# Kernel tuning notes

Hardware: AMD Instinct MI355X
Metric: run time of the kernel (lower is better)

Reference implementation:

```python
import jax, jax.numpy as jnp
import numpy as np

IN_FEATURES = 4096
OUT_FEATURES = 16384
B, S = 8, 16  # small token count -> weight-traffic bound (decode-like)


def setup_inputs() -> dict:
    key = jax.random.key(0)
    k_x, k_w, k_b = jax.random.split(key, 3)
    x = jax.random.normal(k_x, (B, S, IN_FEATURES), dtype=jnp.float32)
    # symmetric int8 quantized weight, values in [-127, 127]
    weight_int = jax.random.randint(k_w, (OUT_FEATURES, IN_FEATURES), -127, 128, dtype=jnp.int32)
    weight_scale = jnp.float32(0.01)      # scalar scale (symmetric, per-tensor)
    weight_zero_point = jnp.float32(0.0)  # symmetric -> zero_point = 0
    bias = jax.random.normal(k_b, (OUT_FEATURES,), dtype=jnp.float32)
    return {"x": x, "weight_int": weight_int, "weight_scale": weight_scale,
            "weight_zero_point": weight_zero_point, "bias": bias}


def reference(x, weight_int, weight_scale, weight_zero_point, bias):
    # dequantize: (q - zp) * scale, then F.linear: x @ W^T + b
    weight_float = (weight_int.astype(jnp.float32) - weight_zero_point) * weight_scale
    # x: [B, S, in], weight_float: [out, in] -> [B, S, out]
    return jnp.einsum('bsi,oi->bso', x, weight_float) + bias
```

## Files before the change

kernel.cpp:

```cpp
#include <hip/hip_runtime.h>
#include <hip/hip_bf16.h>


#define IN_F 4096
#define OUT_F 16384
#define NTOK 128

typedef __attribute__((ext_vector_type(8))) short bf16x8;
typedef __attribute__((ext_vector_type(4))) float f32x4;

__device__ __forceinline__ unsigned short f32_to_bf16_rne(float f) {
  unsigned u = __float_as_uint(f);
  u += 0x7fffu + ((u >> 16) & 1u);
  return (unsigned short)(u >> 16);
}

__global__ __launch_bounds__(512) void prep_x(const float* __restrict__ x,
                                              uint4* __restrict__ xf,
                                              float* __restrict__ xsum) {
  const int token = blockIdx.x;
  const int i = (int)threadIdx.x;
  const int k0 = i << 3;
  const float4 v0 = *(const float4*)(x + token * IN_F + k0);
  const float4 v1 = *(const float4*)(x + token * IN_F + k0 + 4);
  float v[8] = {v0.x, v0.y, v0.z, v0.w, v1.x, v1.y, v1.z, v1.w};
  unsigned short h[8];
  float s = 0.f;
#pragma unroll
  for (int j = 0; j < 8; ++j) {
    s += v[j];
    h[j] = f32_to_bf16_rne(v[j]);
  }
  uint4 o;
  o.x = (unsigned)h[0] | ((unsigned)h[1] << 16);
  o.y = (unsigned)h[2] | ((unsigned)h[3] << 16);
  o.z = (unsigned)h[4] | ((unsigned)h[5] << 16);
  o.w = (unsigned)h[6] | ((unsigned)h[7] << 16);
  const int slab = i >> 2;
  const int q = i & 3;
  const int lane = (q << 4) | (token & 15);
  xf[slab * 512 + (token >> 4) * 64 + lane] = o;

#pragma unroll
  for (int off = 32; off > 0; off >>= 1) s += __shfl_down(s, off, 64);
  __shared__ float wsum[8];
  if ((i & 63) == 0) wsum[i >> 6] = s;
  __syncthreads();
  if (i == 0) {
    float t = 0.f;
#pragma unroll
    for (int a = 0; a < 8; ++a) t += wsum[a];
    xsum[token] = t;
  }
}

__device__ __forceinline__ bf16x8 cvt8(int4 a, int4 b) {
  bf16x8 o;
  o[0] = (short)(__float_as_uint((float)a.x) >> 16);
  o[1] = (short)(__float_as_uint((float)a.y) >> 16);
  o[2] = (short)(__float_as_uint((float)a.z) >> 16);
  o[3] = (short)(__float_as_uint((float)a.w) >> 16);
  o[4] = (short)(__float_as_uint((float)b.x) >> 16);
  o[5] = (short)(__float_as_uint((float)b.y) >> 16);
  o[6] = (short)(__float_as_uint((float)b.z) >> 16);
  o[7] = (short)(__float_as_uint((float)b.w) >> 16);
  return o;
}

__global__ __launch_bounds__(64, 1) void qlinear_main(
    const int* __restrict__ W, const uint4* __restrict__ xf,
    const float* __restrict__ xsum, const float* __restrict__ scale_p,
    const float* __restrict__ zp_p, const float* __restrict__ bias,
    float* __restrict__ out) {
  const int l = (int)threadIdx.x;
  const int q = l >> 4;
  const int r = l & 15;
  const int rt = (int)blockIdx.x;
  const int R0 = rt * 16;

  const int* Wbase = W + (R0 + r) * IN_F + q * 8;
  const int start = (rt * 37) & 127;

  int4 wa[8], wb[8];
  uint4 bb[2][8];

  f32x4 acc[8];
#pragma unroll
  for (int t = 0; t < 8; ++t) acc[t] = (f32x4)0.0f;

#pragma unroll
  for (int d = 0; d < 8; ++d) {
    const int kk = (start + d) & 127;
    wa[d] = *(const int4*)(Wbase + kk * 32);
    wb[d] = *(const int4*)(Wbase + kk * 32 + 4);
  }
#pragma unroll
  for (int d = 0; d < 2; ++d) {
    const int kk = (start + d) & 127;
    const uint4* xp = xf + kk * 512 + l;
#pragma unroll
    for (int t = 0; t < 8; ++t) bb[d][t] = xp[t * 64];
  }

#pragma unroll 1
  for (int k = 0; k <= 112; k += 8) {
#pragma unroll
    for (int u = 0; u < 8; ++u) {
      const int step = k + u;
      {
        const int kk = (start + step + 2) & 127;
        const uint4* xp = xf + kk * 512 + l;
        uint4 nb0 = xp[0 * 64], nb1 = xp[1 * 64], nb2 = xp[2 * 64], nb3 = xp[3 * 64];
        uint4 nb4 = xp[4 * 64], nb5 = xp[5 * 64], nb6 = xp[6 * 64], nb7 = xp[7 * 64];
        const int kw = (start + step + 8) & 127;
        int4 nwa = *(const int4*)(Wbase + kw * 32);
        int4 nwb = *(const int4*)(Wbase + kw * 32 + 4);
        bf16x8 a = cvt8(wa[u], wb[u]);
        wa[u] = nwa;
        wb[u] = nwb;
#pragma unroll
        for (int t = 0; t < 8; ++t) {
          bf16x8 b = *(const bf16x8*)&bb[u & 1][t];
          acc[t] = __builtin_amdgcn_mfma_f32_16x16x32_bf16(a, b, acc[t], 0, 0, 0);
        }
        bb[u & 1][0] = nb0; bb[u & 1][1] = nb1; bb[u & 1][2] = nb2; bb[u & 1][3] = nb3;
        bb[u & 1][4] = nb4; bb[u & 1][5] = nb5; bb[u & 1][6] = nb6; bb[u & 1][7] = nb7;
      }
    }
  }
#pragma unroll
  for (int u = 0; u < 8; ++u) {
    const int step = 120 + u;
    bf16x8 a = cvt8(wa[u], wb[u]);
    if (u < 6) {
      const int kk = (start + step + 2) & 127;
      const uint4* xp = xf + kk * 512 + l;
      uint4 nb[8];
#pragma unroll
      for (int t = 0; t < 8; ++t) nb[t] = xp[t * 64];
#pragma unroll
      for (int t = 0; t < 8; ++t) {
        bf16x8 b = *(const bf16x8*)&bb[u & 1][t];
        acc[t] = __builtin_amdgcn_mfma_f32_16x16x32_bf16(a, b, acc[t], 0, 0, 0);
      }
#pragma unroll
      for (int t = 0; t < 8; ++t) bb[u & 1][t] = nb[t];
    } else {
#pragma unroll
      for (int t = 0; t < 8; ++t) {
        bf16x8 b = *(const bf16x8*)&bb[u & 1][t];
        acc[t] = __builtin_amdgcn_mfma_f32_16x16x32_bf16(a, b, acc[t], 0, 0, 0);
      }
    }
  }

  const float scale = *scale_p;
  const float zp = *zp_p;
  const float czp = scale * zp;
  const float4 bv = *(const float4*)(bias + R0 + q * 4);
#pragma unroll
  for (int t = 0; t < 8; ++t) {
    const int token = t * 16 + r;
    const float corr = -czp * xsum[token];
    float4 o;
    o.x = acc[t][0] * scale + corr + bv.x;
    o.y = acc[t][1] * scale + corr + bv.y;
    o.z = acc[t][2] * scale + corr + bv.z;
    o.w = acc[t][3] * scale + corr + bv.w;
    *(float4*)(out + token * OUT_F + R0 + q * 4) = o;
  }
}

extern "C" void kernel_launch(void* const* d_in, const int* in_sizes, int n_in,
                              void* d_out, int out_size, void* d_ws, size_t ws_size,
                              hipStream_t stream) {
  const float* x = (const float*)d_in[0];
  const int* W = (const int*)d_in[1];
  const float* scale = (const float*)d_in[2];
  const float* zp = (const float*)d_in[3];
  const float* bias = (const float*)d_in[4];
  float* out = (float*)d_out;

  uint4* xf = (uint4*)d_ws;
  float* xsum = (float*)((char*)d_ws + (1 << 20));

  prep_x<<<NTOK, 512, 0, stream>>>(x, xf, xsum);
  qlinear_main<<<OUT_F / 16, 64, 0, stream>>>(W, xf, xsum, scale, zp, bias, out);
}
```

Before: 401.7 us.

## Switch to 32x32 MFMA tiles with split-K across four waves and LDS reduction

The main kernel now gives each block 32 output rows and four waves. Each wave handles a quarter of the K dimension using 32x32x16 bf16 MFMA. Partial accumulators are then reduced through shared memory before the epilogue applies scale, zero-point correction and bias. The x prep layout is reordered to match the new B-operand fragment. The intent is more in-flight weight loads per CU and fewer, larger MFMAs to saturate HBM bandwidth on the int32 weight stream, at the cost of 64KB of LDS per block and a reduction step.

```diff
diff --git a/kernel.cpp b/kernel.cpp
--- a/kernel.cpp
+++ b/kernel.cpp
@@ -8,6 +8,7 @@
 
 typedef __attribute__((ext_vector_type(8))) short bf16x8;
 typedef __attribute__((ext_vector_type(4))) float f32x4;
+typedef __attribute__((ext_vector_type(16))) float f32x16;
 
 __device__ __forceinline__ unsigned short f32_to_bf16_rne(float f) {
   unsigned u = __float_as_uint(f);
@@ -36,10 +37,11 @@
   o.y = (unsigned)h[2] | ((unsigned)h[3] << 16);
   o.z = (unsigned)h[4] | ((unsigned)h[5] << 16);
   o.w = (unsigned)h[6] | ((unsigned)h[7] << 16);
-  const int slab = i >> 2;
-  const int q = i & 3;
-  const int lane = (q << 4) | (token & 15);
-  xf[slab * 512 + (token >> 4) * 64 + lane] = o;
+  const int S = i >> 1;
+  const int half = i & 1;
+  const int t = token >> 5;
+  const int lane = half * 32 + (token & 31);
+  xf[(S * 4 + t) * 64 + lane] = o;
 
 #pragma unroll
   for (int off = 32; off > 0; off >>= 1) s += __shfl_down(s, off, 64);
@@ -47,10 +49,10 @@
   if ((i & 63) == 0) wsum[i >> 6] = s;
   __syncthreads();
   if (i == 0) {
-    float t = 0.f;
-#pragma unroll
-    for (int a = 0; a < 8; ++a) t += wsum[a];
-    xsum[token] = t;
+    float t2 = 0.f;
+#pragma unroll
+    for (int a = 0; a < 8; ++a) t2 += wsum[a];
+    xsum[token] = t2;
   }
 }
 
@@ -67,107 +69,125 @@
   return o;
 }
 
-__global__ __launch_bounds__(64, 1) void qlinear_main(
+__global__ __launch_bounds__(256, 2) void qlinear_main(
     const int* __restrict__ W, const uint4* __restrict__ xf,
     const float* __restrict__ xsum, const float* __restrict__ scale_p,
     const float* __restrict__ zp_p, const float* __restrict__ bias,
     float* __restrict__ out) {
-  const int l = (int)threadIdx.x;
-  const int q = l >> 4;
-  const int r = l & 15;
+  __shared__ f32x4 red[4 * 1024];
+
+  const int tid = (int)threadIdx.x;
+  const int w = tid >> 6;
+  const int l = tid & 63;
+  const int row = l & 31;
+  const int hb = l >> 5;
   const int rt = (int)blockIdx.x;
-  const int R0 = rt * 16;
-
-  const int* Wbase = W + (R0 + r) * IN_F + q * 8;
-  const int start = (rt * 37) & 127;
+  const int R0 = rt * 32;
+
+  const int* Wbase = W + (R0 + row) * IN_F + w * 1024 + hb * 8;
+  const uint4* xfb = xf + l;
+  const int s0 = (rt * 13) & 63;
 
   int4 wa[8], wb[8];
-  uint4 bb[2][8];
-
-  f32x4 acc[8];
-#pragma unroll
-  for (int t = 0; t < 8; ++t) acc[t] = (f32x4)0.0f;
+  uint4 bb[2][4];
+
+  f32x16 acc[4];
+#pragma unroll
+  for (int t = 0; t < 4; ++t) acc[t] = (f32x16)0.0f;
 
 #pragma unroll
   for (int d = 0; d < 8; ++d) {
-    const int kk = (start + d) & 127;
-    wa[d] = *(const int4*)(Wbase + kk * 32);
-    wb[d] = *(const int4*)(Wbase + kk * 32 + 4);
+    const int ss = (s0 + d) & 63;
+    wa[d] = *(const int4*)(Wbase + ss * 16);
+    wb[d] = *(const int4*)(Wbase + ss * 16 + 4);
   }
 #pragma unroll
   for (int d = 0; d < 2; ++d) {
-    const int kk = (start + d) & 127;
-    const uint4* xp = xf + kk * 512 + l;
-#pragma unroll
-    for (int t = 0; t < 8; ++t) bb[d][t] = xp[t * 64];
+    const int S = w * 64 + ((s0 + d) & 63);
+#pragma unroll
+    for (int t = 0; t < 4; ++t) bb[d][t] = xfb[(S * 4 + t) * 64];
   }
 
 #pragma unroll 1
-  for (int k = 0; k <= 112; k += 8) {
+  for (int it = 0; it < 7; ++it) {
 #pragma unroll
     for (int u = 0; u < 8; ++u) {
-      const int step = k + u;
-      {
-        const int kk = (start + step + 2) & 127;
-        const uint4* xp = xf + kk * 512 + l;
-        uint4 nb0 = xp[0 * 64], nb1 = xp[1 * 64], nb2 = xp[2 * 64], nb3 = xp[3 * 64];
-        uint4 nb4 = xp[4 * 64], nb5 = xp[5 * 64], nb6 = xp[6 * 64], nb7 = xp[7 * 64];
-        const int kw = (start + step + 8) & 127;
-        int4 nwa = *(const int4*)(Wbase + kw * 32);
-        int4 nwb = *(const int4*)(Wbase + kw * 32 + 4);
-        bf16x8 a = cvt8(wa[u], wb[u]);
-        wa[u] = nwa;
-        wb[u] = nwb;
-#pragma unroll
-        for (int t = 0; t < 8; ++t) {
-          bf16x8 b = *(const bf16x8*)&bb[u & 1][t];
-          acc[t] = __builtin_amdgcn_mfma_f32_16x16x32_bf16(a, b, acc[t], 0, 0, 0);
-        }
-        bb[u & 1][0] = nb0; bb[u & 1][1] = nb1; bb[u & 1][2] = nb2; bb[u & 1][3] = nb3;
-        bb[u & 1][4] = nb4; bb[u & 1][5] = nb5; bb[u & 1][6] = nb6; bb[u & 1][7] = nb7;
-      }
+      const int s = it * 8 + u;
+      const int Sn = w * 64 + ((s0 + s + 2) & 63);
+      uint4 nb0 = xfb[(Sn * 4 + 0) * 64];
+      uint4 nb1 = xfb[(Sn * 4 + 1) * 64];
+      uint4 nb2 = xfb[(Sn * 4 + 2) * 64];
+      uint4 nb3 = xfb[(Sn * 4 + 3) * 64];
+      const int ssw = (s0 + s + 8) & 63;
+      int4 nwa = *(const int4*)(Wbase + ssw * 16);
+      int4 nwb = *(const int4*)(Wbase + ssw * 16 + 4);
+      bf16x8 a = cvt8(wa[u], wb[u]);
+      acc[0] = __builtin_amdgcn_mfma_f32_32x32x16_bf16(a, *(const bf16x8*)&bb[u & 1][0], acc[0], 0, 0, 0);
+      acc[1] = __builtin_amdgcn_mfma_f32_32x32x16_bf16(a, *(const bf16x8*)&bb[u & 1][1], acc[1], 0, 0, 0);
+      acc[2] = __builtin_amdgcn_mfma_f32_32x32x16_bf16(a, *(const bf16x8*)&bb[u & 1][2], acc[2], 0, 0, 0);
+      acc[3] = __builtin_amdgcn_mfma_f32_32x32x16_bf16(a, *(const bf16x8*)&bb[u & 1][3], acc[3], 0, 0, 0);
+      wa[u] = nwa; wb[u] = nwb;
+      bb[u & 1][0] = nb0; bb[u & 1][1] = nb1; bb[u & 1][2] = nb2; bb[u & 1][3] = nb3;
     }
   }
 #pragma unroll
   for (int u = 0; u < 8; ++u) {
-    const int step = 120 + u;
+    const int s = 56 + u;
     bf16x8 a = cvt8(wa[u], wb[u]);
     if (u < 6) {
-      const int kk = (start + step + 2) & 127;
-      const uint4* xp = xf + kk * 512 + l;
-      uint4 nb[8];
-#pragma unroll
-      for (int t = 0; t < 8; ++t) nb[t] = xp[t * 64];
-#pragma unroll
-      for (int t = 0; t < 8; ++t) {
-        bf16x8 b = *(const bf16x8*)&bb[u & 1][t];
-        acc[t] = __builtin_amdgcn_mfma_f32_16x16x32_bf16(a, b, acc[t], 0, 0, 0);
-      }
-#pragma unroll
-      for (int t = 0; t < 8; ++t) bb[u & 1][t] = nb[t];
+      const int Sn = w * 64 + ((s0 + s + 2) & 63);
+      uint4 nb0 = xfb[(Sn * 4 + 0) * 64];
+      uint4 nb1 = xfb[(Sn * 4 + 1) * 64];
+      uint4 nb2 = xfb[(Sn * 4 + 2) * 64];
+      uint4 nb3 = xfb[(Sn * 4 + 3) * 64];
+      acc[0] = __builtin_amdgcn_mfma_f32_32x32x16_bf16(a, *(const bf16x8*)&bb[u & 1][0], acc[0], 0, 0, 0);
+      acc[1] = __builtin_amdgcn_mfma_f32_32x32x16_bf16(a, *(const bf16x8*)&bb[u & 1][1], acc[1], 0, 0, 0);
+      acc[2] = __builtin_amdgcn_mfma_f32_32x32x16_bf16(a, *(const bf16x8*)&bb[u & 1][2], acc[2], 0, 0, 0);
+      acc[3] = __builtin_amdgcn_mfma_f32_32x32x16_bf16(a, *(const bf16x8*)&bb[u & 1][3], acc[3], 0, 0, 0);
+      bb[u & 1][0] = nb0; bb[u & 1][1] = nb1; bb[u & 1][2] = nb2; bb[u & 1][3] = nb3;
     } else {
-#pragma unroll
-      for (int t = 0; t < 8; ++t) {
-        bf16x8 b = *(const bf16x8*)&bb[u & 1][t];
-        acc[t] = __builtin_amdgcn_mfma_f32_16x16x32_bf16(a, b, acc[t], 0, 0, 0);
-      }
+      acc[0] = __builtin_amdgcn_mfma_f32_32x32x16_bf16(a, *(const bf16x8*)&bb[u & 1][0], acc[0], 0, 0, 0);
+      acc[1] = __builtin_amdgcn_mfma_f32_32x32x16_bf16(a, *(const bf16x8*)&bb[u & 1][1], acc[1], 0, 0, 0);
+      acc[2] = __builtin_amdgcn_mfma_f32_32x32x16_bf16(a, *(const bf16x8*)&bb[u & 1][2], acc[2], 0, 0, 0);
+      acc[3] = __builtin_amdgcn_mfma_f32_32x32x16_bf16(a, *(const bf16x8*)&bb[u & 1][3], acc[3], 0, 0, 0);
     }
   }
+
+#pragma unroll
+  for (int t = 0; t < 4; ++t)
+#pragma unroll
+    for (int g = 0; g < 4; ++g) {
+      f32x4 v;
+      v[0] = acc[t][g * 4 + 0]; v[1] = acc[t][g * 4 + 1];
+      v[2] = acc[t][g * 4 + 2]; v[3] = acc[t][g * 4 + 3];
+      red[w * 1024 + (t * 4 + g) * 64 + l] = v;
+    }
+  __syncthreads();
 
   const float scale = *scale_p;
   const float zp = *zp_p;
   const float czp = scale * zp;
-  const float4 bv = *(const float4*)(bias + R0 + q * 4);
-#pragma unroll
-  for (int t = 0; t < 8; ++t) {
-    const int token = t * 16 + r;
+#pragma unroll
+  for (int j = 0; j < 4; ++j) {
+    const int c = j * 256 + tid;
+    const int chunk = c >> 6;
+    const int ln = c & 63;
+    f32x4 sum = red[chunk * 64 + ln] + red[1024 + chunk * 64 + ln] +
+                red[2048 + chunk * 64 + ln] + red[3072 + chunk * 64 + ln];
+    const int t = chunk >> 2;
+    const int g = chunk & 3;
+    const int col = ln & 31;
+    const int half = ln >> 5;
+    const int token = t * 32 + col;
+    const int feat = R0 + 8 * g + 4 * half;
     const float corr = -czp * xsum[token];
+    const float4 bv = *(const float4*)(bias + feat);
     float4 o;
-    o.x = acc[t][0] * scale + corr + bv.x;
-    o.y = acc[t][1] * scale + corr + bv.y;
-    o.z = acc[t][2] * scale + corr + bv.z;
-    o.w = acc[t][3] * scale + corr + bv.w;
-    *(float4*)(out + token * OUT_F + R0 + q * 4) = o;
+    o.x = sum[0] * scale + corr + bv.x;
+    o.y = sum[1] * scale + corr + bv.y;
+    o.z = sum[2] * scale + corr + bv.z;
+    o.w = sum[3] * scale + corr + bv.w;
+    *(float4*)(out + token * OUT_F + feat) = o;
   }
 }
 
@@ -185,5 +205,5 @@
   float* xsum = (float*)((char*)d_ws + (1 << 20));
 
   prep_x<<<NTOK, 512, 0, stream>>>(x, xf, xsum);
-  qlinear_main<<<OUT_F / 16, 64, 0, stream>>>(W, xf, xsum, scale, zp, bias, out);
-}
+  qlinear_main<<<OUT_F / 32, 256, 0, stream>>>(W, xf, xsum, scale, zp, bias, out);
+}
```

Result: faster. 385.8 us (-4.0%).
